# Kernel optimization log

Hardware: AMD Instinct MI355X
Metric: run time of the kernel (lower is better)

Reference implementation:

```python
import jax, jax.numpy as jnp
import numpy as np

Z, H, M, N, Y = 128, 512, 256, 10, 4   # z_size, hidden, mem_vec, mem_size, y_dim
B, T = 2048, 32
SHIFT_IND = np.concatenate([np.roll(np.arange(N), s) for s in (-1, 0, 1)])  # [3*N]


def setup_inputs() -> dict:
    key = jax.random.key(0)
    ks = iter(jax.random.split(key, 48))
    def nrm(shape, s=0.05):
        return jax.random.normal(next(ks), shape, dtype=jnp.float32) * s
    d = {}
    d["z_seq"] = jax.random.normal(next(ks), (B, T, Z), dtype=jnp.float32)
    d["W_ih"] = nrm((4 * H, Z + M)); d["W_hh"] = nrm((4 * H, H))
    d["b_ih"] = jnp.zeros((4 * H,), jnp.float32); d["b_hh"] = jnp.zeros((4 * H,), jnp.float32)
    heads = {"read_key": M, "write_key": M, "erase": M, "add": M, "y": Y,
             "rks": 1, "wks": 1, "rig": 1, "wig": 1, "rsh": 3, "wsh": 3, "rshp": 1, "wshp": 1}
    for nm, o in heads.items():
        d["W_" + nm] = nrm((o, H)); d["b_" + nm] = jnp.zeros((o,), jnp.float32)
    d["memory_init"] = nrm((N, M))
    d["gamma"] = jnp.ones((Z,), jnp.float32)
    d["beta"] = jnp.zeros((Z,), jnp.float32)
    return d


def reference(z_seq, W_ih, W_hh, b_ih, b_hh,
              W_read_key, b_read_key, W_write_key, b_write_key,
              W_erase, b_erase, W_add, b_add, W_y, b_y,
              W_rks, b_rks, W_wks, b_wks, W_rig, b_rig, W_wig, b_wig,
              W_rsh, b_rsh, W_wsh, b_wsh, W_rshp, b_rshp, W_wshp, b_wshp,
              memory_init, gamma, beta):
    Bs, Ts = z_seq.shape[0], z_seq.shape[1]
    eps = 1e-8
    # context norm over the time axis (single task segment), unbiased var as torch
    mu = z_seq.mean(1, keepdims=True)
    sig = jnp.sqrt(z_seq.var(1, ddof=1, keepdims=True) + eps)
    z = (z_seq - mu) / sig * gamma + beta
    z_ext = jnp.concatenate([z, jnp.zeros((Bs, 1, Z), z.dtype)], axis=1)  # t == T step uses zero input
    shift_ind = jnp.asarray(SHIFT_IND)

    def lin(h, W, b):
        return h @ W.T + b

    def cos_sim(key_v, mem):  # key [B,M], mem [B,N,M] -> [B,N]
        dot = jnp.einsum('bm,bnm->bn', key_v, mem)
        kn = jnp.maximum(jnp.linalg.norm(key_v, axis=1, keepdims=True), eps)
        mn = jnp.maximum(jnp.linalg.norm(mem, axis=2), eps)
        return dot / (kn * mn)

    def address(key_v, strength, gate, shift_w, sharpen, w_prev, mem, use_interp):
        # content addressing (exp(s*sim)/sum == softmax), interpolation, circular shift, sharpening
        w = jax.nn.softmax(strength * cos_sim(key_v, mem), axis=1)      # [B,N]
        w = jnp.where(use_interp, gate * w + (1.0 - gate) * w_prev, w)
        w_sh = w[:, shift_ind].reshape(Bs, 3, N)                        # gather per shift
        w = jnp.einsum('bsn,bs->bn', w_sh, shift_w)
        wp = w ** sharpen
        return wp / wp.sum(1, keepdims=True)

    def step(carry, xs):
        h, c, read_vec, mem, w_read, w_write = carry
        z_t, t = xs
        lstm_in = jnp.concatenate([z_t, read_vec], axis=1)              # [B, Z+M]
        gates = lstm_in @ W_ih.T + b_ih + h @ W_hh.T + b_hh
        i, f, g, o = jnp.split(gates, 4, axis=1)
        c = jax.nn.sigmoid(f) * c + jax.nn.sigmoid(i) * jnp.tanh(g)
        h = jax.nn.sigmoid(o) * jnp.tanh(c)
        read_key = jnp.tanh(lin(h, W_read_key, b_read_key))
        write_key = jnp.tanh(lin(h, W_write_key, b_write_key))
        rks = jax.nn.softplus(lin(h, W_rks, b_rks))
        wks = jax.nn.softplus(lin(h, W_wks, b_wks))
        rig = jax.nn.sigmoid(lin(h, W_rig, b_rig))
        wig = jax.nn.sigmoid(lin(h, W_wig, b_wig))
        rsh = jax.nn.softmax(lin(h, W_rsh, b_rsh), axis=1)
        wsh = jax.nn.softmax(lin(h, W_wsh, b_wsh), axis=1)
        rshp = jax.nn.softplus(lin(h, W_rshp, b_rshp)) + 1.0
        wshp = jax.nn.softplus(lin(h, W_wshp, b_wshp)) + 1.0
        erase = jax.nn.sigmoid(lin(h, W_erase, b_erase))
        add = jnp.tanh(lin(h, W_add, b_add))
        y_lin = lin(h, W_y, b_y)
        # read (skipped at t==0; interpolation only for t>1)
        w_read_new = address(read_key, rks, rig, rsh, rshp, w_read, mem, t > 1)
        read_vec = jnp.where(t == 0, jnp.zeros((Bs, M), z_t.dtype),
                             jnp.einsum('bnm,bn->bm', mem, w_read_new))
        w_read = jnp.where(t == 0, w_read, w_read_new)
        # write (every step; interpolation only for t>0)
        w_write = address(write_key, wks, wig, wsh, wshp, w_write, mem, t > 0)
        ww = w_write[:, :, None]
        mem = mem * (1.0 - erase[:, None, :] * ww) + add[:, None, :] * ww
        return (h, c, read_vec, mem, w_read, w_write), y_lin

    carry0 = (jnp.zeros((Bs, H), z.dtype), jnp.zeros((Bs, H), z.dtype),
              jnp.zeros((Bs, M), z.dtype),
              jnp.broadcast_to(memory_init, (Bs, N, M)).astype(z.dtype),
              jnp.zeros((Bs, N), z.dtype), jnp.zeros((Bs, N), z.dtype))
    ts = jnp.arange(Ts + 1)
    _, ys = jax.lax.scan(step, carry0, (jnp.swapaxes(z_ext, 0, 1), ts))
    y_pred_linear = ys[-1]  # output of the final (t == T) step
    return y_pred_linear, jnp.argmax(y_pred_linear, axis=1)
```

## Files before the change

kernel.cpp:

```cpp
#include <hip/hip_runtime.h>
#include <hip/hip_bf16.h>

typedef __attribute__((ext_vector_type(8))) short short8;
typedef __attribute__((ext_vector_type(4))) float f32x4;

#define Bsz   2048
#define Tsz   32
#define Zsz   128
#define Hsz   512
#define Msz   256
#define Nsz   10
#define KDIM  896
#define NGATE 2048
#define NHEAD 1040
#define NHEADP 1152

#define ACT_S ((size_t)Bsz * 768)
#define ZPL_S ((size_t)33 * Bsz * 128)
#define WG_S  ((size_t)NGATE * KDIM)
#define WH_S  ((size_t)NHEADP * Hsz)

__device__ __forceinline__ float sigmoidf_(float x) { return 1.f / (1.f + expf(-x)); }
__device__ __forceinline__ float softplusf_(float x) { return x > 20.f ? x : log1pf(expf(x)); }

__device__ __forceinline__ float wave_sum(float v) {
#pragma unroll
    for (int m = 32; m >= 1; m >>= 1) v += __shfl_xor(v, m, 64);
    return v;
}

__device__ __forceinline__ void split3(float v, __hip_bfloat16& o1, __hip_bfloat16& o2, __hip_bfloat16& o3) {
    o1 = __float2bfloat16(v);
    float r = v - __bfloat162float(o1);
    o2 = __float2bfloat16(r);
    r -= __bfloat162float(o2);
    o3 = __float2bfloat16(r);
}

__device__ __forceinline__ void split3u(float v, unsigned short& a, unsigned short& b, unsigned short& c) {
    __hip_bfloat16 x, y, z;
    split3(v, x, y, z);
    a = *reinterpret_cast<unsigned short*>(&x);
    b = *reinterpret_cast<unsigned short*>(&y);
    c = *reinterpret_cast<unsigned short*>(&z);
}

#define MFMA16(A, B, C) __builtin_amdgcn_mfma_f32_16x16x32_bf16((A), (B), (C), 0, 0, 0)

__device__ __forceinline__ void gload16(const void* g, void* l) {
    __builtin_amdgcn_global_load_lds(
        (const __attribute__((address_space(1))) void*)g,
        (__attribute__((address_space(3))) void*)l, 16, 0, 0);
}


__global__ __launch_bounds__(256) void k_lnorm(
    const float* __restrict__ z_seq, const float* __restrict__ gamma,
    const float* __restrict__ beta, __hip_bfloat16* __restrict__ zb)
{
    int idx = blockIdx.x * 256 + threadIdx.x;
    if (idx >= Bsz * Zsz) return;
    int b = idx >> 7, zi = idx & 127;
    const float* p = z_seq + (size_t)b * Tsz * Zsz + zi;
    float v[32];
    float s = 0.f;
#pragma unroll
    for (int t = 0; t < Tsz; t++) { v[t] = p[t * Zsz]; s += v[t]; }
    float mu = s * (1.f / 32.f);
    float ss = 0.f;
#pragma unroll
    for (int t = 0; t < Tsz; t++) { float d = v[t] - mu; ss += d * d; }
    float rs = rsqrtf(ss * (1.f / 31.f) + 1e-8f);
    float ga = gamma[zi], be = beta[zi];
#pragma unroll
    for (int t = 0; t <= Tsz; t++) {
        float val = (t < Tsz) ? (v[t] - mu) * rs * ga + be : 0.f;
        __hip_bfloat16 a, bq, c;
        split3(val, a, bq, c);
        size_t o = ((size_t)t * Bsz + b) * 128 + zi;
        zb[o] = a; zb[o + ZPL_S] = bq; zb[o + 2 * ZPL_S] = c;
    }
}

__global__ __launch_bounds__(256) void k_prep_wcat(
    const float* __restrict__ W_ih, const float* __restrict__ W_hh,
    const float* __restrict__ b_ih, const float* __restrict__ b_hh,
    __hip_bfloat16* __restrict__ Wt, float* __restrict__ bcat)
{
    int idx = blockIdx.x * 256 + threadIdx.x;
    if (idx >= NGATE * KDIM) return;
    int n = idx / KDIM, k = idx % KDIM;
    int jl = n & 15, g = (n >> 4) & 3, jg = n >> 6;
    int r = g * Hsz + jg * 16 + jl;
    float v = (k < 384) ? W_ih[(size_t)r * 384 + k] : W_hh[(size_t)r * Hsz + (k - 384)];
    __hip_bfloat16 a, b, c;
    split3(v, a, b, c);
    Wt[idx] = a; Wt[idx + WG_S] = b; Wt[idx + 2 * WG_S] = c;
    if (k == 0) bcat[n] = b_ih[r] + b_hh[r];
}

struct HeadP { const float* W[13]; const float* b[13]; };

__global__ __launch_bounds__(256) void k_prep_heads(
    HeadP hp, __hip_bfloat16* __restrict__ Wt, float* __restrict__ bh)
{
    int idx = blockIdx.x * 256 + threadIdx.x;
    if (idx >= NHEADP * Hsz) return;
    int n = idx / Hsz, k = idx % Hsz;
    float v = 0.f;
    if (n < NHEAD) {
        const int offs[14] = {0,256,512,768,1024,1028,1029,1030,1031,1032,1035,1038,1039,1040};
        int h = 0;
        while (n >= offs[h + 1]) h++;
        int local = n - offs[h];
        v = hp.W[h][(size_t)local * Hsz + k];
        if (k == 0) bh[n] = hp.b[h][local];
    } else if (k == 0) bh[n] = 0.f;
    __hip_bfloat16 a, b, c;
    split3(v, a, b, c);
    Wt[idx] = a; Wt[idx + WH_S] = b; Wt[idx + 2 * WH_S] = c;
}

__global__ __launch_bounds__(256) void k_init(
    __hip_bfloat16* __restrict__ act,
    float* __restrict__ cbuf, float* __restrict__ w_read, float* __restrict__ w_write,
    float* __restrict__ mem, const float* __restrict__ memory_init)
{
    int tid = blockIdx.x * blockDim.x + threadIdx.x;
    int stride = gridDim.x * blockDim.x;
    const __hip_bfloat16 z0 = __float2bfloat16(0.f);
    for (size_t i = tid; i < 6 * ACT_S; i += stride) act[i] = z0;
    for (int i = tid; i < Bsz * Hsz; i += stride) cbuf[i] = 0.f;
    for (int i = tid; i < Bsz * Nsz; i += stride) { w_read[i] = 0.f; w_write[i] = 0.f; }
    for (int i = tid; i < Bsz * Nsz * Msz; i += stride) mem[i] = memory_init[i % (Nsz * Msz)];
}


__device__ __forceinline__ void stage_tile(
    uint8_t* smem, int wid, int lane,
    const __hip_bfloat16* aP0, size_t aPlaneStride, int aRowStride, int aColOff, int row0,
    const __hip_bfloat16* bP0, size_t bPlaneStride, int bRowStride, int n00,
    int k0)
{
    const int row4 = lane >> 2;
    const int sch = (lane & 3) ^ (row4 & 3);
    const int koff = sch << 3;
#pragma unroll
    for (int i = 0; i < 9; ++i) {
        int c = wid * 9 + i;
        if (c < 24) {
            int p = c >> 3, rg = c & 7;
            int row = rg * 16 + row4;
            const __hip_bfloat16* g = aP0 + (size_t)p * aPlaneStride +
                (size_t)(row0 + row) * aRowStride + aColOff + k0 + koff;
            gload16(g, smem + p * 8192 + rg * 1024);
        } else {
            int c2 = c - 24;
            int p = c2 >> 2, rg = c2 & 3;
            int row = rg * 16 + row4;
            const __hip_bfloat16* g = bP0 + (size_t)p * bPlaneStride +
                (size_t)(n00 + row) * bRowStride + k0 + koff;
            gload16(g, smem + 24576 + p * 4096 + rg * 1024);
        }
    }
}

__global__ __launch_bounds__(256, 2) void k_gates(
    const __hip_bfloat16* __restrict__ zt,
    const __hip_bfloat16* __restrict__ actin,
    const __hip_bfloat16* __restrict__ Wg,
    const float* __restrict__ bcat,
    float* __restrict__ cbuf,
    __hip_bfloat16* __restrict__ actout)
{
    __shared__ __align__(1024) uint8_t smem[36864];
    const int tid = threadIdx.x;
    const int wid = tid >> 6, lane = tid & 63;
    const int fr = lane & 15, kg = lane >> 4;
    const int wr = wid >> 1, wc = wid & 1;
    const int wg = blockIdx.x;
    const int xcd = wg & 7, rr = wg >> 3;
    const int bm = (xcd & 1) * 8 + (rr & 7);
    const int bn = (xcd >> 1) * 8 + (rr >> 3);
    const int row0 = bm * 128, n00 = bn * 64;

    f32x4 acc[4][2];
#pragma unroll
    for (int s = 0; s < 4; ++s)
#pragma unroll
        for (int u = 0; u < 2; ++u) acc[s][u] = f32x4{0.f, 0.f, 0.f, 0.f};

    const int swz = (kg ^ (fr & 3)) << 4;
    constexpr int PA[6] = {0, 0, 1, 0, 1, 2};
    constexpr int PB[6] = {0, 1, 0, 2, 1, 0};

    const int NKT = KDIM / 32;
    for (int kt = 0; kt < NKT; ++kt) {
        const int k0 = kt * 32;
        if (k0 < 128)
            stage_tile(smem, wid, lane, zt, ZPL_S, 128, 0, row0, Wg, WG_S, KDIM, n00, k0);
        else
            stage_tile(smem, wid, lane, actin, ACT_S, 768, -128, row0, Wg, WG_S, KDIM, n00, k0);
        __syncthreads();

        short8 af[3][4];
#pragma unroll
        for (int p = 0; p < 3; ++p)
#pragma unroll
            for (int s = 0; s < 4; ++s)
                af[p][s] = *(const short8*)(smem + p * 8192 + (wr * 64 + s * 16 + fr) * 64 + swz);
        short8 bf[3][2];
#pragma unroll
        for (int p = 0; p < 3; ++p)
#pragma unroll
            for (int u = 0; u < 2; ++u)
                bf[p][u] = *(const short8*)(smem + 24576 + p * 4096 + (wc * 32 + u * 16 + fr) * 64 + swz);

#pragma unroll
        for (int pr = 0; pr < 6; ++pr)
#pragma unroll
            for (int s = 0; s < 4; ++s)
#pragma unroll
                for (int u = 0; u < 2; ++u)
                    acc[s][u] = MFMA16(af[PA[pr]][s], bf[PB[pr]][u], acc[s][u]);
        __syncthreads();
    }

    float* G = (float*)smem;
#pragma unroll
    for (int s = 0; s < 4; ++s)
#pragma unroll
        for (int u = 0; u < 2; ++u) {
            int g = wc * 2 + u;
#pragma unroll
            for (int r = 0; r < 4; ++r) {
                int row = wr * 64 + s * 16 + kg * 4 + r;
                G[(g * 128 + row) * 17 + fr] = acc[s][u][r];
            }
        }
    __syncthreads();

#pragma unroll
    for (int i = 0; i < 8; ++i) {
        int p2 = i * 256 + tid;
        int row = p2 >> 4, jl = p2 & 15;
        int m = row0 + row;
        int j = bn * 16 + jl;
        float iv = G[(0 * 128 + row) * 17 + jl] + bcat[n00 +  0 + jl];
        float fv = G[(1 * 128 + row) * 17 + jl] + bcat[n00 + 16 + jl];
        float gv = G[(2 * 128 + row) * 17 + jl] + bcat[n00 + 32 + jl];
        float ov = G[(3 * 128 + row) * 17 + jl] + bcat[n00 + 48 + jl];
        size_t ci = (size_t)m * Hsz + j;
        float co = cbuf[ci];
        float cn = sigmoidf_(fv) * co + sigmoidf_(iv) * tanhf(gv);
        float hn = sigmoidf_(ov) * tanhf(cn);
        cbuf[ci] = cn;
        __hip_bfloat16 h1, h2, h3;
        split3(hn, h1, h2, h3);
        size_t ho = (size_t)m * 768 + 256 + j;
        actout[ho] = h1; actout[ho + ACT_S] = h2; actout[ho + 2 * ACT_S] = h3;
    }
}

__global__ __launch_bounds__(256, 2) void k_heads(
    const __hip_bfloat16* __restrict__ actout,
    const __hip_bfloat16* __restrict__ Wh,
    const float* __restrict__ bh,
    float* __restrict__ headbuf,
    int nOff)
{
    __shared__ __align__(1024) uint8_t smem[36864];
    const int tid = threadIdx.x;
    const int wid = tid >> 6, lane = tid & 63;
    const int fr = lane & 15, kg = lane >> 4;
    const int wr = wid >> 1, wc = wid & 1;
    const int bm = blockIdx.x, bn = blockIdx.y + nOff;
    const int row0 = bm * 128, n00 = bn * 64;

    f32x4 acc[4][2];
#pragma unroll
    for (int s = 0; s < 4; ++s)
#pragma unroll
        for (int u = 0; u < 2; ++u) acc[s][u] = f32x4{0.f, 0.f, 0.f, 0.f};

    const int swz = (kg ^ (fr & 3)) << 4;
    constexpr int PA[6] = {0, 0, 1, 0, 1, 2};
    constexpr int PB[6] = {0, 1, 0, 2, 1, 0};

    const int NKT = Hsz / 32;
    for (int kt = 0; kt < NKT; ++kt) {
        stage_tile(smem, wid, lane, actout, ACT_S, 768, 256, row0, Wh, WH_S, Hsz, n00, kt * 32);
        __syncthreads();

        short8 af[3][4];
#pragma unroll
        for (int p = 0; p < 3; ++p)
#pragma unroll
            for (int s = 0; s < 4; ++s)
                af[p][s] = *(const short8*)(smem + p * 8192 + (wr * 64 + s * 16 + fr) * 64 + swz);
        short8 bf[3][2];
#pragma unroll
        for (int p = 0; p < 3; ++p)
#pragma unroll
            for (int u = 0; u < 2; ++u)
                bf[p][u] = *(const short8*)(smem + 24576 + p * 4096 + (wc * 32 + u * 16 + fr) * 64 + swz);

#pragma unroll
        for (int pr = 0; pr < 6; ++pr)
#pragma unroll
            for (int s = 0; s < 4; ++s)
#pragma unroll
                for (int u = 0; u < 2; ++u)
                    acc[s][u] = MFMA16(af[PA[pr]][s], bf[PB[pr]][u], acc[s][u]);
        __syncthreads();
    }

#pragma unroll
    for (int s = 0; s < 4; ++s)
#pragma unroll
        for (int u = 0; u < 2; ++u) {
            int n = n00 + wc * 32 + u * 16 + fr;
            if (n >= NHEAD) continue;
            float bias = bh[n];
#pragma unroll
            for (int r = 0; r < 4; ++r) {
                int m = row0 + wr * 64 + s * 16 + kg * 4 + r;
                headbuf[(size_t)m * NHEAD + n] = acc[s][u][r] + bias;
            }
        }
}


__device__ inline void compute_address(
    const float dot[10], const float mn[10], float kn, float strength, float gate,
    const float sh[3], float sharp, const float* __restrict__ wprev, bool interp,
    float out[10])
{
    float w[10];
    float mx = -1e30f;
#pragma unroll
    for (int n = 0; n < 10; n++) {
        w[n] = strength * (dot[n] / (kn * mn[n]));
        mx = fmaxf(mx, w[n]);
    }
    float s = 0.f;
#pragma unroll
    for (int n = 0; n < 10; n++) { w[n] = expf(w[n] - mx); s += w[n]; }
    float inv = 1.f / s;
#pragma unroll
    for (int n = 0; n < 10; n++) w[n] *= inv;
    if (interp) {
#pragma unroll
        for (int n = 0; n < 10; n++) w[n] = gate * w[n] + (1.f - gate) * wprev[n];
    }
    float w2[10];
#pragma unroll
    for (int n = 0; n < 10; n++) {
        int np1 = (n + 1) % 10, nm1 = (n + 9) % 10;
        w2[n] = sh[0] * w[np1] + sh[1] * w[n] + sh[2] * w[nm1];
    }
    float ssum = 0.f;
#pragma unroll
    for (int n = 0; n < 10; n++) { w2[n] = powf(w2[n], sharp); ssum += w2[n]; }
    float rinv = 1.f / ssum;
#pragma unroll
    for (int n = 0; n < 10; n++) out[n] = w2[n] * rinv;
}

__global__ __launch_bounds__(64) void k_addr3(
    const float* __restrict__ headbuf,
    float* __restrict__ mem,
    float* __restrict__ w_read, float* __restrict__ w_write,
    __hip_bfloat16* __restrict__ actout,
    int t)
{
    const int b = blockIdx.x;
    const int lane = threadIdx.x;
    const float eps = 1e-8f;
    const float* hb = headbuf + (size_t)b * NHEAD;
    float* memb = mem + (size_t)b * Nsz * Msz;

    float4 rk = *reinterpret_cast<const float4*>(hb + lane * 4);
    float4 wk = *reinterpret_cast<const float4*>(hb + 256 + lane * 4);
    float4 er = *reinterpret_cast<const float4*>(hb + 512 + lane * 4);
    float4 ad = *reinterpret_cast<const float4*>(hb + 768 + lane * 4);
    float4 mreg[10];
#pragma unroll
    for (int n = 0; n < 10; n++)
        mreg[n] = *reinterpret_cast<const float4*>(memb + n * Msz + lane * 4);

    rk.x = tanhf(rk.x); rk.y = tanhf(rk.y); rk.z = tanhf(rk.z); rk.w = tanhf(rk.w);
    wk.x = tanhf(wk.x); wk.y = tanhf(wk.y); wk.z = tanhf(wk.z); wk.w = tanhf(wk.w);
    er.x = sigmoidf_(er.x); er.y = sigmoidf_(er.y); er.z = sigmoidf_(er.z); er.w = sigmoidf_(er.w);
    ad.x = tanhf(ad.x); ad.y = tanhf(ad.y); ad.z = tanhf(ad.z); ad.w = tanhf(ad.w);

    float knr = fmaxf(sqrtf(wave_sum(rk.x*rk.x + rk.y*rk.y + rk.z*rk.z + rk.w*rk.w)), eps);
    float knw = fmaxf(sqrtf(wave_sum(wk.x*wk.x + wk.y*wk.y + wk.z*wk.z + wk.w*wk.w)), eps);

    float dotr[10], dotw[10], mn[10];
#pragma unroll
    for (int n = 0; n < 10; n++) {
        float4 m4 = mreg[n];
        dotr[n] = wave_sum(rk.x*m4.x + rk.y*m4.y + rk.z*m4.z + rk.w*m4.w);
        dotw[n] = wave_sum(wk.x*m4.x + wk.y*m4.y + wk.z*m4.z + wk.w*m4.w);
        mn[n]   = fmaxf(sqrtf(wave_sum(m4.x*m4.x + m4.y*m4.y + m4.z*m4.z + m4.w*m4.w)), eps);
    }

    float rks = softplusf_(hb[1028]);
    float wks = softplusf_(hb[1029]);
    float rig = sigmoidf_(hb[1030]);
    float wig = sigmoidf_(hb[1031]);
    float rsh[3], wsh[3];
    {
        float a0 = hb[1032], a1 = hb[1033], a2 = hb[1034];
        float mx = fmaxf(a0, fmaxf(a1, a2));
        float e0 = expf(a0 - mx), e1 = expf(a1 - mx), e2 = expf(a2 - mx);
        float inv = 1.f / (e0 + e1 + e2);
        rsh[0] = e0 * inv; rsh[1] = e1 * inv; rsh[2] = e2 * inv;
        a0 = hb[1035]; a1 = hb[1036]; a2 = hb[1037];
        mx = fmaxf(a0, fmaxf(a1, a2));
        e0 = expf(a0 - mx); e1 = expf(a1 - mx); e2 = expf(a2 - mx);
        inv = 1.f / (e0 + e1 + e2);
        wsh[0] = e0 * inv; wsh[1] = e1 * inv; wsh[2] = e2 * inv;
    }
    float rshp = softplusf_(hb[1038]) + 1.f;
    float wshp = softplusf_(hb[1039]) + 1.f;

    float wfr[10], wfw[10];
    compute_address(dotr, mn, knr, rks, rig, rsh, rshp, w_read + (size_t)b * Nsz, t > 1, wfr);
    compute_address(dotw, mn, knw, wks, wig, wsh, wshp, w_write + (size_t)b * Nsz, t > 0, wfw);

    {
        float4 rv = {0.f, 0.f, 0.f, 0.f};
#pragma unroll
        for (int n = 0; n < 10; n++) {
            float wn = wfr[n];
            rv.x += mreg[n].x * wn; rv.y += mreg[n].y * wn;
            rv.z += mreg[n].z * wn; rv.w += mreg[n].w * wn;
        }
        if (t == 0) rv = float4{0.f, 0.f, 0.f, 0.f};
        ushort4 u1, u2, u3;
        split3u(rv.x, u1.x, u2.x, u3.x);
        split3u(rv.y, u1.y, u2.y, u3.y);
        split3u(rv.z, u1.z, u2.z, u3.z);
        split3u(rv.w, u1.w, u2.w, u3.w);
        size_t o = (size_t)b * 768 + lane * 4;
        *reinterpret_cast<ushort4*>(actout + o)             = u1;
        *reinterpret_cast<ushort4*>(actout + o + ACT_S)     = u2;
        *reinterpret_cast<ushort4*>(actout + o + 2 * ACT_S) = u3;
    }
    if (lane < 10) {
        if (t != 0) w_read[(size_t)b * Nsz + lane] = wfr[lane];
        w_write[(size_t)b * Nsz + lane] = wfw[lane];
    }
#pragma unroll
    for (int n = 0; n < 10; n++) {
        float wwn = wfw[n];
        float4 m4 = mreg[n];
        float4 o4;
        o4.x = m4.x * (1.f - er.x * wwn) + ad.x * wwn;
        o4.y = m4.y * (1.f - er.y * wwn) + ad.y * wwn;
        o4.z = m4.z * (1.f - er.z * wwn) + ad.z * wwn;
        o4.w = m4.w * (1.f - er.w * wwn) + ad.w * wwn;
        *reinterpret_cast<float4*>(memb + n * Msz + lane * 4) = o4;
    }
}

__global__ __launch_bounds__(64) void k_out(
    const float* __restrict__ headbuf, float* __restrict__ d_out)
{
    int b = blockIdx.x * 64 + threadIdx.x;
    if (b >= Bsz) return;
    float4 y = *reinterpret_cast<const float4*>(headbuf + (size_t)b * NHEAD + 1024);
    d_out[(size_t)b * 4 + 0] = y.x;
    d_out[(size_t)b * 4 + 1] = y.y;
    d_out[(size_t)b * 4 + 2] = y.z;
    d_out[(size_t)b * 4 + 3] = y.w;
    int idx = 0; float best = y.x;
    if (y.y > best) { best = y.y; idx = 1; }
    if (y.z > best) { best = y.z; idx = 2; }
    if (y.w > best) { best = y.w; idx = 3; }
    d_out[Bsz * 4 + b] = (float)idx;
}


extern "C" void kernel_launch(void* const* d_in, const int* in_sizes, int n_in,
                              void* d_out, int out_size, void* d_ws, size_t ws_size,
                              hipStream_t stream) {
    const float* z_seq = (const float*)d_in[0];
    const float* W_ih  = (const float*)d_in[1];
    const float* W_hh  = (const float*)d_in[2];
    const float* b_ih  = (const float*)d_in[3];
    const float* b_hh  = (const float*)d_in[4];
    const float* memory_init = (const float*)d_in[31];
    const float* gamma = (const float*)d_in[32];
    const float* beta  = (const float*)d_in[33];

    HeadP hp;
    for (int i = 0; i < 13; i++) {
        hp.W[i] = (const float*)d_in[5 + 2 * i];
        hp.b[i] = (const float*)d_in[6 + 2 * i];
    }

    char* ws = (char*)d_ws;
    size_t off = 0;
    auto alloc = [&](size_t bytes) -> void* {
        off = (off + 255) & ~(size_t)255;
        void* p = ws + off;
        off += bytes;
        return p;
    };
    __hip_bfloat16* zbuf  = (__hip_bfloat16*)alloc(3 * ZPL_S * 2);
    __hip_bfloat16* act   = (__hip_bfloat16*)alloc(2 * 3 * ACT_S * 2);
    float* cbuf    = (float*)alloc((size_t)Bsz * Hsz * 4);
    float* mem     = (float*)alloc((size_t)Bsz * Nsz * Msz * 4);
    float* w_read  = (float*)alloc((size_t)Bsz * Nsz * 4);
    float* w_write = (float*)alloc((size_t)Bsz * Nsz * 4);
    float* headbuf = (float*)alloc((size_t)Bsz * NHEAD * 4);
    __hip_bfloat16* Wg = (__hip_bfloat16*)alloc(3 * WG_S * 2);
    float* bcat    = (float*)alloc((size_t)NGATE * 4);
    __hip_bfloat16* Wh = (__hip_bfloat16*)alloc(3 * WH_S * 2);
    float* bhead   = (float*)alloc((size_t)NHEADP * 4);

    k_prep_wcat<<<(NGATE * KDIM + 255) / 256, 256, 0, stream>>>(W_ih, W_hh, b_ih, b_hh, Wg, bcat);
    k_prep_heads<<<(NHEADP * Hsz + 255) / 256, 256, 0, stream>>>(hp, Wh, bhead);
    k_lnorm<<<(Bsz * Zsz + 255) / 256, 256, 0, stream>>>(z_seq, gamma, beta, zbuf);
    k_init<<<2048, 256, 0, stream>>>(act, cbuf, w_read, w_write, mem, memory_init);

    float* out_f = (float*)d_out;
    for (int t = 0; t < Tsz; t++) {
        const __hip_bfloat16* ain = act + (size_t)(t & 1) * 3 * ACT_S;
        __hip_bfloat16*       aout = act + (size_t)((t + 1) & 1) * 3 * ACT_S;
        k_gates<<<512, 256, 0, stream>>>(
            zbuf + (size_t)t * Bsz * 128, ain, Wg, bcat, cbuf, aout);
        k_heads<<<dim3(16, 18), 256, 0, stream>>>(aout, Wh, bhead, headbuf, 0);
        k_addr3<<<Bsz, 64, 0, stream>>>(headbuf, mem, w_read, w_write, aout, t);
    }
    {
        const int t = Tsz;
        const __hip_bfloat16* ain = act + (size_t)(t & 1) * 3 * ACT_S;
        __hip_bfloat16*       aout = act + (size_t)((t + 1) & 1) * 3 * ACT_S;
        k_gates<<<512, 256, 0, stream>>>(
            zbuf + (size_t)t * Bsz * 128, ain, Wg, bcat, cbuf, aout);
        k_heads<<<dim3(16, 1), 256, 0, stream>>>(aout, Wh, bhead, headbuf, 16);
        k_out<<<Bsz / 64, 64, 0, stream>>>(headbuf, out_f);
    }
}
```

Baseline: 3.409 ms.

## Split memory addressing kernel across four waves per batch row

The per-batch addressing kernel now runs 256 threads (four wavefronts) per batch element instead of one. Each wave holds two or three memory slots, computes partial dot products and norms, and exchanges them through shared memory. Wave 0 then computes the addressing weights, and all waves apply the erase/add update and partial read vectors, which are reduced in shared memory. The goal is more parallelism and fewer serial wave reductions per wave, at the cost of three block barriers and idle waves during the serial addressing step.

```diff
diff --git a/kernel.cpp b/kernel.cpp
--- a/kernel.cpp
+++ b/kernel.cpp
@@ -367,7 +367,7 @@
     for (int n = 0; n < 10; n++) out[n] = w2[n] * rinv;
 }
 
-__global__ __launch_bounds__(64) void k_addr3(
+__global__ __launch_bounds__(256) void k_addr4(
     const float* __restrict__ headbuf,
     float* __restrict__ mem,
     float* __restrict__ w_read, float* __restrict__ w_write,
@@ -375,69 +375,128 @@
     int t)
 {
     const int b = blockIdx.x;
-    const int lane = threadIdx.x;
+    const int tid = threadIdx.x;
+    const int wid = tid >> 6, lane = tid & 63;
     const float eps = 1e-8f;
     const float* hb = headbuf + (size_t)b * NHEAD;
     float* memb = mem + (size_t)b * Nsz * Msz;
+
+    __shared__ float fin[32];
+    __shared__ float W2[20];
+    __shared__ float4 Prv[4][64];
 
     float4 rk = *reinterpret_cast<const float4*>(hb + lane * 4);
     float4 wk = *reinterpret_cast<const float4*>(hb + 256 + lane * 4);
     float4 er = *reinterpret_cast<const float4*>(hb + 512 + lane * 4);
     float4 ad = *reinterpret_cast<const float4*>(hb + 768 + lane * 4);
-    float4 mreg[10];
-#pragma unroll
-    for (int n = 0; n < 10; n++)
-        mreg[n] = *reinterpret_cast<const float4*>(memb + n * Msz + lane * 4);
+
+    const int nc = (wid < 2) ? 3 : 2;
+    float4 mreg[3];
+#pragma unroll 3
+    for (int i = 0; i < 3; ++i) {
+        if (i < nc) {
+            int n = wid + i * 4;
+            mreg[i] = *reinterpret_cast<const float4*>(memb + n * Msz + lane * 4);
+        }
+    }
 
     rk.x = tanhf(rk.x); rk.y = tanhf(rk.y); rk.z = tanhf(rk.z); rk.w = tanhf(rk.w);
     wk.x = tanhf(wk.x); wk.y = tanhf(wk.y); wk.z = tanhf(wk.z); wk.w = tanhf(wk.w);
     er.x = sigmoidf_(er.x); er.y = sigmoidf_(er.y); er.z = sigmoidf_(er.z); er.w = sigmoidf_(er.w);
     ad.x = tanhf(ad.x); ad.y = tanhf(ad.y); ad.z = tanhf(ad.z); ad.w = tanhf(ad.w);
 
-    float knr = fmaxf(sqrtf(wave_sum(rk.x*rk.x + rk.y*rk.y + rk.z*rk.z + rk.w*rk.w)), eps);
-    float knw = fmaxf(sqrtf(wave_sum(wk.x*wk.x + wk.y*wk.y + wk.z*wk.z + wk.w*wk.w)), eps);
-
-    float dotr[10], dotw[10], mn[10];
-#pragma unroll
-    for (int n = 0; n < 10; n++) {
-        float4 m4 = mreg[n];
-        dotr[n] = wave_sum(rk.x*m4.x + rk.y*m4.y + rk.z*m4.z + rk.w*m4.w);
-        dotw[n] = wave_sum(wk.x*m4.x + wk.y*m4.y + wk.z*m4.z + wk.w*m4.w);
-        mn[n]   = fmaxf(sqrtf(wave_sum(m4.x*m4.x + m4.y*m4.y + m4.z*m4.z + m4.w*m4.w)), eps);
-    }
-
-    float rks = softplusf_(hb[1028]);
-    float wks = softplusf_(hb[1029]);
-    float rig = sigmoidf_(hb[1030]);
-    float wig = sigmoidf_(hb[1031]);
-    float rsh[3], wsh[3];
-    {
-        float a0 = hb[1032], a1 = hb[1033], a2 = hb[1034];
-        float mx = fmaxf(a0, fmaxf(a1, a2));
-        float e0 = expf(a0 - mx), e1 = expf(a1 - mx), e2 = expf(a2 - mx);
-        float inv = 1.f / (e0 + e1 + e2);
-        rsh[0] = e0 * inv; rsh[1] = e1 * inv; rsh[2] = e2 * inv;
-        a0 = hb[1035]; a1 = hb[1036]; a2 = hb[1037];
-        mx = fmaxf(a0, fmaxf(a1, a2));
-        e0 = expf(a0 - mx); e1 = expf(a1 - mx); e2 = expf(a2 - mx);
-        inv = 1.f / (e0 + e1 + e2);
-        wsh[0] = e0 * inv; wsh[1] = e1 * inv; wsh[2] = e2 * inv;
-    }
-    float rshp = softplusf_(hb[1038]) + 1.f;
-    float wshp = softplusf_(hb[1039]) + 1.f;
-
-    float wfr[10], wfw[10];
-    compute_address(dotr, mn, knr, rks, rig, rsh, rshp, w_read + (size_t)b * Nsz, t > 1, wfr);
-    compute_address(dotw, mn, knw, wks, wig, wsh, wshp, w_write + (size_t)b * Nsz, t > 0, wfw);
-
-    {
-        float4 rv = {0.f, 0.f, 0.f, 0.f};
+#pragma unroll 3
+    for (int i = 0; i < 3; ++i) {
+        if (i < nc) {
+            int n = wid + i * 4;
+            float4 m4 = mreg[i];
+            float dr = wave_sum(rk.x*m4.x + rk.y*m4.y + rk.z*m4.z + rk.w*m4.w);
+            float dw = wave_sum(wk.x*m4.x + wk.y*m4.y + wk.z*m4.z + wk.w*m4.w);
+            float m2 = wave_sum(m4.x*m4.x + m4.y*m4.y + m4.z*m4.z + m4.w*m4.w);
+            if (lane == 0) { fin[n] = dr; fin[10 + n] = dw; fin[20 + n] = m2; }
+        }
+    }
+    if (wid == 0) {
+        float k2r = wave_sum(rk.x*rk.x + rk.y*rk.y + rk.z*rk.z + rk.w*rk.w);
+        if (lane == 0) fin[30] = k2r;
+    } else if (wid == 1) {
+        float k2w = wave_sum(wk.x*wk.x + wk.y*wk.y + wk.z*wk.z + wk.w*wk.w);
+        if (lane == 0) fin[31] = k2w;
+    }
+    __syncthreads();
+
+    if (wid == 0) {
+        float dotr[10], dotw[10], mn[10];
 #pragma unroll
         for (int n = 0; n < 10; n++) {
-            float wn = wfr[n];
-            rv.x += mreg[n].x * wn; rv.y += mreg[n].y * wn;
-            rv.z += mreg[n].z * wn; rv.w += mreg[n].w * wn;
-        }
+            dotr[n] = fin[n];
+            dotw[n] = fin[10 + n];
+            mn[n] = fmaxf(sqrtf(fin[20 + n]), eps);
+        }
+        const float knr = fmaxf(sqrtf(fin[30]), eps);
+        const float knw = fmaxf(sqrtf(fin[31]), eps);
+
+        float rks = softplusf_(hb[1028]);
+        float wks = softplusf_(hb[1029]);
+        float rig = sigmoidf_(hb[1030]);
+        float wig = sigmoidf_(hb[1031]);
+        float rsh[3], wsh[3];
+        {
+            float a0 = hb[1032], a1 = hb[1033], a2 = hb[1034];
+            float mx = fmaxf(a0, fmaxf(a1, a2));
+            float e0 = expf(a0 - mx), e1 = expf(a1 - mx), e2 = expf(a2 - mx);
+            float inv = 1.f / (e0 + e1 + e2);
+            rsh[0] = e0 * inv; rsh[1] = e1 * inv; rsh[2] = e2 * inv;
+            a0 = hb[1035]; a1 = hb[1036]; a2 = hb[1037];
+            mx = fmaxf(a0, fmaxf(a1, a2));
+            e0 = expf(a0 - mx); e1 = expf(a1 - mx); e2 = expf(a2 - mx);
+            inv = 1.f / (e0 + e1 + e2);
+            wsh[0] = e0 * inv; wsh[1] = e1 * inv; wsh[2] = e2 * inv;
+        }
+        float rshp = softplusf_(hb[1038]) + 1.f;
+        float wshp = softplusf_(hb[1039]) + 1.f;
+
+        float wfr[10], wfw[10];
+        compute_address(dotr, mn, knr, rks, rig, rsh, rshp, w_read + (size_t)b * Nsz, t > 1, wfr);
+        compute_address(dotw, mn, knw, wks, wig, wsh, wshp, w_write + (size_t)b * Nsz, t > 0, wfw);
+
+        if (lane < 10) {
+            W2[lane] = wfr[lane];
+            W2[10 + lane] = wfw[lane];
+            if (t != 0) w_read[(size_t)b * Nsz + lane] = wfr[lane];
+            w_write[(size_t)b * Nsz + lane] = wfw[lane];
+        }
+    }
+    __syncthreads();
+
+    float4 rvp = {0.f, 0.f, 0.f, 0.f};
+#pragma unroll 3
+    for (int i = 0; i < 3; ++i) {
+        if (i < nc) {
+            int n = wid + i * 4;
+            float wfrn = W2[n];
+            float wwn = W2[10 + n];
+            float4 m4 = mreg[i];
+            rvp.x += m4.x * wfrn; rvp.y += m4.y * wfrn;
+            rvp.z += m4.z * wfrn; rvp.w += m4.w * wfrn;
+            float4 o4;
+            o4.x = m4.x * (1.f - er.x * wwn) + ad.x * wwn;
+            o4.y = m4.y * (1.f - er.y * wwn) + ad.y * wwn;
+            o4.z = m4.z * (1.f - er.z * wwn) + ad.z * wwn;
+            o4.w = m4.w * (1.f - er.w * wwn) + ad.w * wwn;
+            *reinterpret_cast<float4*>(memb + n * Msz + lane * 4) = o4;
+        }
+    }
+    Prv[wid][lane] = rvp;
+    __syncthreads();
+
+    if (wid == 0) {
+        float4 p0 = Prv[0][lane], p1 = Prv[1][lane], p2 = Prv[2][lane], p3 = Prv[3][lane];
+        float4 rv;
+        rv.x = (p0.x + p1.x) + (p2.x + p3.x);
+        rv.y = (p0.y + p1.y) + (p2.y + p3.y);
+        rv.z = (p0.z + p1.z) + (p2.z + p3.z);
+        rv.w = (p0.w + p1.w) + (p2.w + p3.w);
         if (t == 0) rv = float4{0.f, 0.f, 0.f, 0.f};
         ushort4 u1, u2, u3;
         split3u(rv.x, u1.x, u2.x, u3.x);
@@ -448,21 +507,6 @@
         *reinterpret_cast<ushort4*>(actout + o)             = u1;
         *reinterpret_cast<ushort4*>(actout + o + ACT_S)     = u2;
         *reinterpret_cast<ushort4*>(actout + o + 2 * ACT_S) = u3;
-    }
-    if (lane < 10) {
-        if (t != 0) w_read[(size_t)b * Nsz + lane] = wfr[lane];
-        w_write[(size_t)b * Nsz + lane] = wfw[lane];
-    }
-#pragma unroll
-    for (int n = 0; n < 10; n++) {
-        float wwn = wfw[n];
-        float4 m4 = mreg[n];
-        float4 o4;
-        o4.x = m4.x * (1.f - er.x * wwn) + ad.x * wwn;
-        o4.y = m4.y * (1.f - er.y * wwn) + ad.y * wwn;
-        o4.z = m4.z * (1.f - er.z * wwn) + ad.z * wwn;
-        o4.w = m4.w * (1.f - er.w * wwn) + ad.w * wwn;
-        *reinterpret_cast<float4*>(memb + n * Msz + lane * 4) = o4;
     }
 }
 
@@ -534,7 +578,7 @@
         k_gates<<<512, 256, 0, stream>>>(
             zbuf + (size_t)t * Bsz * 128, ain, Wg, bcat, cbuf, aout);
         k_heads<<<dim3(16, 18), 256, 0, stream>>>(aout, Wh, bhead, headbuf, 0);
-        k_addr3<<<Bsz, 64, 0, stream>>>(headbuf, mem, w_read, w_write, aout, t);
+        k_addr4<<<Bsz, 256, 0, stream>>>(headbuf, mem, w_read, w_write, aout, t);
     }
     {
         const int t = Tsz;
```

After: 3.764 ms. 10.4% more time.

## Fuse per-step kernels into one persistent cooperative kernel with grid syncs

Applied to the files above, without the earlier changes.

Replaces the per-timestep launches of the gates, heads and addressing kernels with a single cooperative persistent kernel. Stages are separated by grid-wide barriers, and the blocks loop over the tiles and rows of each stage. This removes roughly a hundred kernel launches and their launch gaps. In exchange it adds grid-sync costs, and the addressing stage packs four 64-lane rows into each 256-thread block at the GEMM kernel's occupancy. The old multi-launch path is kept as a fallback if the cooperative launch fails.

```diff
diff --git a/kernel.cpp b/kernel.cpp
--- a/kernel.cpp
+++ b/kernel.cpp
@@ -1,5 +1,8 @@
 #include <hip/hip_runtime.h>
 #include <hip/hip_bf16.h>
+#include <hip/hip_cooperative_groups.h>
+
+namespace cg = cooperative_groups;
 
 typedef __attribute__((ext_vector_type(8))) short short8;
 typedef __attribute__((ext_vector_type(4))) float f32x4;
@@ -165,7 +168,8 @@
     }
 }
 
-__global__ __launch_bounds__(256, 2) void k_gates(
+__device__ void gates_tile(
+    uint8_t* smem, int wg,
     const __hip_bfloat16* __restrict__ zt,
     const __hip_bfloat16* __restrict__ actin,
     const __hip_bfloat16* __restrict__ Wg,
@@ -173,12 +177,10 @@
     float* __restrict__ cbuf,
     __hip_bfloat16* __restrict__ actout)
 {
-    __shared__ __align__(1024) uint8_t smem[36864];
     const int tid = threadIdx.x;
     const int wid = tid >> 6, lane = tid & 63;
     const int fr = lane & 15, kg = lane >> 4;
     const int wr = wid >> 1, wc = wid & 1;
-    const int wg = blockIdx.x;
     const int xcd = wg & 7, rr = wg >> 3;
     const int bm = (xcd & 1) * 8 + (rr & 7);
     const int bn = (xcd >> 1) * 8 + (rr >> 3);
@@ -260,21 +262,21 @@
         size_t ho = (size_t)m * 768 + 256 + j;
         actout[ho] = h1; actout[ho + ACT_S] = h2; actout[ho + 2 * ACT_S] = h3;
     }
-}
-
-__global__ __launch_bounds__(256, 2) void k_heads(
+    __syncthreads();
+}
+
+__device__ void heads_tile(
+    uint8_t* smem,
     const __hip_bfloat16* __restrict__ actout,
     const __hip_bfloat16* __restrict__ Wh,
     const float* __restrict__ bh,
     float* __restrict__ headbuf,
-    int nOff)
-{
-    __shared__ __align__(1024) uint8_t smem[36864];
+    int bm, int bn)
+{
     const int tid = threadIdx.x;
     const int wid = tid >> 6, lane = tid & 63;
     const int fr = lane & 15, kg = lane >> 4;
     const int wr = wid >> 1, wc = wid & 1;
-    const int bm = blockIdx.x, bn = blockIdx.y + nOff;
     const int row0 = bm * 128, n00 = bn * 64;
 
     f32x4 acc[4][2];
@@ -328,10 +330,10 @@
                 headbuf[(size_t)m * NHEAD + n] = acc[s][u][r] + bias;
             }
         }
-}
-
-
-__device__ inline void compute_address(
+    __syncthreads();
+}
+
+__device__ void compute_address(
     const float dot[10], const float mn[10], float kn, float strength, float gate,
     const float sh[3], float sharp, const float* __restrict__ wprev, bool interp,
     float out[10])
@@ -367,15 +369,13 @@
     for (int n = 0; n < 10; n++) out[n] = w2[n] * rinv;
 }
 
-__global__ __launch_bounds__(64) void k_addr3(
+__device__ void addr_row(
     const float* __restrict__ headbuf,
     float* __restrict__ mem,
     float* __restrict__ w_read, float* __restrict__ w_write,
     __hip_bfloat16* __restrict__ actout,
-    int t)
-{
-    const int b = blockIdx.x;
-    const int lane = threadIdx.x;
+    int t, int b, int lane)
+{
     const float eps = 1e-8f;
     const float* hb = headbuf + (size_t)b * NHEAD;
     float* memb = mem + (size_t)b * Nsz * Msz;
@@ -466,6 +466,32 @@
     }
 }
 
+
+__global__ __launch_bounds__(256, 2) void k_gates(
+    const __hip_bfloat16* __restrict__ zt, const __hip_bfloat16* __restrict__ actin,
+    const __hip_bfloat16* __restrict__ Wg, const float* __restrict__ bcat,
+    float* __restrict__ cbuf, __hip_bfloat16* __restrict__ actout)
+{
+    __shared__ __align__(1024) uint8_t smem[36864];
+    gates_tile(smem, blockIdx.x, zt, actin, Wg, bcat, cbuf, actout);
+}
+
+__global__ __launch_bounds__(256, 2) void k_heads(
+    const __hip_bfloat16* __restrict__ actout, const __hip_bfloat16* __restrict__ Wh,
+    const float* __restrict__ bh, float* __restrict__ headbuf, int nOff)
+{
+    __shared__ __align__(1024) uint8_t smem[36864];
+    heads_tile(smem, actout, Wh, bh, headbuf, blockIdx.x, blockIdx.y + nOff);
+}
+
+__global__ __launch_bounds__(64) void k_addr3(
+    const float* __restrict__ headbuf, float* __restrict__ mem,
+    float* __restrict__ w_read, float* __restrict__ w_write,
+    __hip_bfloat16* __restrict__ actout, int t)
+{
+    addr_row(headbuf, mem, w_read, w_write, actout, t, blockIdx.x, threadIdx.x);
+}
+
 __global__ __launch_bounds__(64) void k_out(
     const float* __restrict__ headbuf, float* __restrict__ d_out)
 {
@@ -481,6 +507,70 @@
     if (y.z > best) { best = y.z; idx = 2; }
     if (y.w > best) { best = y.w; idx = 3; }
     d_out[Bsz * 4 + b] = (float)idx;
+}
+
+
+__global__ __launch_bounds__(256, 2) void k_step_all(
+    const __hip_bfloat16* __restrict__ zbuf,
+    __hip_bfloat16* __restrict__ act,
+    const __hip_bfloat16* __restrict__ Wg,
+    const float* __restrict__ bcat,
+    float* __restrict__ cbuf,
+    const __hip_bfloat16* __restrict__ Wh,
+    const float* __restrict__ bhead,
+    float* __restrict__ headbuf,
+    float* __restrict__ mem,
+    float* __restrict__ w_read,
+    float* __restrict__ w_write,
+    float* __restrict__ d_out)
+{
+    cg::grid_group grid = cg::this_grid();
+    __shared__ __align__(1024) uint8_t smem[36864];
+    const int tid = threadIdx.x;
+    const int wid = tid >> 6, lane = tid & 63;
+    const int bid = blockIdx.x;
+    const int nb = gridDim.x;
+
+    for (int t = 0; t <= Tsz; ++t) {
+        const __hip_bfloat16* ain = act + (size_t)(t & 1) * 3 * ACT_S;
+        __hip_bfloat16*       aout = act + (size_t)((t + 1) & 1) * 3 * ACT_S;
+        const __hip_bfloat16* zt = zbuf + (size_t)t * Bsz * 128;
+
+        for (int wg = bid; wg < 512; wg += nb)
+            gates_tile(smem, wg, zt, ain, Wg, bcat, cbuf, aout);
+        __threadfence();
+        grid.sync();
+
+        if (t < Tsz) {
+            for (int i = bid; i < 288; i += nb)
+                heads_tile(smem, aout, Wh, bhead, headbuf, i & 15, i >> 4);
+            __threadfence();
+            grid.sync();
+
+            for (int r = bid * 4 + wid; r < Bsz; r += nb * 4)
+                addr_row(headbuf, mem, w_read, w_write, aout, t, r, lane);
+            __threadfence();
+            grid.sync();
+        } else {
+            for (int i = bid; i < 16; i += nb)
+                heads_tile(smem, aout, Wh, bhead, headbuf, i, 16);
+            __threadfence();
+            grid.sync();
+
+            for (int b = bid * 256 + tid; b < Bsz; b += nb * 256) {
+                float4 y = *reinterpret_cast<const float4*>(headbuf + (size_t)b * NHEAD + 1024);
+                d_out[(size_t)b * 4 + 0] = y.x;
+                d_out[(size_t)b * 4 + 1] = y.y;
+                d_out[(size_t)b * 4 + 2] = y.z;
+                d_out[(size_t)b * 4 + 3] = y.w;
+                int idx = 0; float best = y.x;
+                if (y.y > best) { best = y.y; idx = 1; }
+                if (y.z > best) { best = y.z; idx = 2; }
+                if (y.w > best) { best = y.w; idx = 3; }
+                d_out[Bsz * 4 + b] = (float)idx;
+            }
+        }
+    }
 }
 
 
@@ -528,15 +618,33 @@
     k_init<<<2048, 256, 0, stream>>>(act, cbuf, w_read, w_write, mem, memory_init);
 
     float* out_f = (float*)d_out;
-    for (int t = 0; t < Tsz; t++) {
-        const __hip_bfloat16* ain = act + (size_t)(t & 1) * 3 * ACT_S;
-        __hip_bfloat16*       aout = act + (size_t)((t + 1) & 1) * 3 * ACT_S;
-        k_gates<<<512, 256, 0, stream>>>(
-            zbuf + (size_t)t * Bsz * 128, ain, Wg, bcat, cbuf, aout);
-        k_heads<<<dim3(16, 18), 256, 0, stream>>>(aout, Wh, bhead, headbuf, 0);
-        k_addr3<<<Bsz, 64, 0, stream>>>(headbuf, mem, w_read, w_write, aout, t);
-    }
-    {
+
+    int maxActive = 0;
+    hipError_t qe = hipOccupancyMaxActiveBlocksPerMultiprocessor(
+        &maxActive, (const void*)k_step_all, 256, 0);
+    bool coop_done = false;
+    if (qe == hipSuccess && maxActive >= 1) {
+        int nblk = (maxActive >= 2) ? 512 : 256;
+        void* args[] = {
+            (void*)&zbuf, (void*)&act, (void*)&Wg, (void*)&bcat, (void*)&cbuf,
+            (void*)&Wh, (void*)&bhead, (void*)&headbuf, (void*)&mem,
+            (void*)&w_read, (void*)&w_write, (void*)&out_f
+        };
+        hipError_t le = hipLaunchCooperativeKernel((const void*)k_step_all,
+                                                   dim3(nblk), dim3(256), args, 0, stream);
+        if (le == hipSuccess) coop_done = true;
+        else (void)hipGetLastError();
+    }
+
+    if (!coop_done) {
+        for (int t = 0; t < Tsz; t++) {
+            const __hip_bfloat16* ain = act + (size_t)(t & 1) * 3 * ACT_S;
+            __hip_bfloat16*       aout = act + (size_t)((t + 1) & 1) * 3 * ACT_S;
+            k_gates<<<512, 256, 0, stream>>>(
+                zbuf + (size_t)t * Bsz * 128, ain, Wg, bcat, cbuf, aout);
+            k_heads<<<dim3(16, 18), 256, 0, stream>>>(aout, Wh, bhead, headbuf, 0);
+            k_addr3<<<Bsz, 64, 0, stream>>>(headbuf, mem, w_read, w_write, aout, t);
+        }
         const int t = Tsz;
         const __hip_bfloat16* ain = act + (size_t)(t & 1) * 3 * ACT_S;
         __hip_bfloat16*       aout = act + (size_t)((t + 1) & 1) * 3 * ACT_S;
```

New measurement: 4.878 ms. 43.1% more time.

## Skip zero-state GEMM work at first step, drop act zeroing, swizzle heads tiles

Applied to the files above, without the earlier changes.

At t=0 the gates GEMM runs only over the z input columns (4 k-tiles), because the recurrent state and read vector are zero then. This lets the initial zero-fill of the activation buffers be dropped. The heads kernel also remaps block indices so tiles sharing operands land on the same XCD, aiming for better L2 reuse. The risk is that any activation region later read without being written first, such as the read-vector slice of the second buffer, now holds uninitialised data.

```diff
diff --git a/kernel.cpp b/kernel.cpp
--- a/kernel.cpp
+++ b/kernel.cpp
@@ -122,14 +122,11 @@
 }
 
 __global__ __launch_bounds__(256) void k_init(
-    __hip_bfloat16* __restrict__ act,
     float* __restrict__ cbuf, float* __restrict__ w_read, float* __restrict__ w_write,
     float* __restrict__ mem, const float* __restrict__ memory_init)
 {
     int tid = blockIdx.x * blockDim.x + threadIdx.x;
     int stride = gridDim.x * blockDim.x;
-    const __hip_bfloat16 z0 = __float2bfloat16(0.f);
-    for (size_t i = tid; i < 6 * ACT_S; i += stride) act[i] = z0;
     for (int i = tid; i < Bsz * Hsz; i += stride) cbuf[i] = 0.f;
     for (int i = tid; i < Bsz * Nsz; i += stride) { w_read[i] = 0.f; w_write[i] = 0.f; }
     for (int i = tid; i < Bsz * Nsz * Msz; i += stride) mem[i] = memory_init[i % (Nsz * Msz)];
@@ -165,6 +162,7 @@
     }
 }
 
+template<int NKT>
 __global__ __launch_bounds__(256, 2) void k_gates(
     const __hip_bfloat16* __restrict__ zt,
     const __hip_bfloat16* __restrict__ actin,
@@ -194,7 +192,6 @@
     constexpr int PA[6] = {0, 0, 1, 0, 1, 2};
     constexpr int PB[6] = {0, 1, 0, 2, 1, 0};
 
-    const int NKT = KDIM / 32;
     for (int kt = 0; kt < NKT; ++kt) {
         const int k0 = kt * 32;
         if (k0 < 128)
@@ -274,7 +271,16 @@
     const int wid = tid >> 6, lane = tid & 63;
     const int fr = lane & 15, kg = lane >> 4;
     const int wr = wid >> 1, wc = wid & 1;
-    const int bm = blockIdx.x, bn = blockIdx.y + nOff;
+    int bm, bn;
+    if (nOff == 0) {
+        int lin = blockIdx.y * 16 + blockIdx.x;
+        int swz = (lin & 7) * 36 + (lin >> 3);
+        bm = swz & 15;
+        bn = swz >> 4;
+    } else {
+        bm = blockIdx.x;
+        bn = nOff;
+    }
     const int row0 = bm * 128, n00 = bn * 64;
 
     f32x4 acc[4][2];
@@ -283,7 +289,7 @@
 #pragma unroll
         for (int u = 0; u < 2; ++u) acc[s][u] = f32x4{0.f, 0.f, 0.f, 0.f};
 
-    const int swz = (kg ^ (fr & 3)) << 4;
+    const int swzl = (kg ^ (fr & 3)) << 4;
     constexpr int PA[6] = {0, 0, 1, 0, 1, 2};
     constexpr int PB[6] = {0, 1, 0, 2, 1, 0};
 
@@ -297,13 +303,13 @@
         for (int p = 0; p < 3; ++p)
 #pragma unroll
             for (int s = 0; s < 4; ++s)
-                af[p][s] = *(const short8*)(smem + p * 8192 + (wr * 64 + s * 16 + fr) * 64 + swz);
+                af[p][s] = *(const short8*)(smem + p * 8192 + (wr * 64 + s * 16 + fr) * 64 + swzl);
         short8 bf[3][2];
 #pragma unroll
         for (int p = 0; p < 3; ++p)
 #pragma unroll
             for (int u = 0; u < 2; ++u)
-                bf[p][u] = *(const short8*)(smem + 24576 + p * 4096 + (wc * 32 + u * 16 + fr) * 64 + swz);
+                bf[p][u] = *(const short8*)(smem + 24576 + p * 4096 + (wc * 32 + u * 16 + fr) * 64 + swzl);
 
 #pragma unroll
         for (int pr = 0; pr < 6; ++pr)
@@ -525,14 +531,18 @@
     k_prep_wcat<<<(NGATE * KDIM + 255) / 256, 256, 0, stream>>>(W_ih, W_hh, b_ih, b_hh, Wg, bcat);
     k_prep_heads<<<(NHEADP * Hsz + 255) / 256, 256, 0, stream>>>(hp, Wh, bhead);
     k_lnorm<<<(Bsz * Zsz + 255) / 256, 256, 0, stream>>>(z_seq, gamma, beta, zbuf);
-    k_init<<<2048, 256, 0, stream>>>(act, cbuf, w_read, w_write, mem, memory_init);
+    k_init<<<2048, 256, 0, stream>>>(cbuf, w_read, w_write, mem, memory_init);
 
     float* out_f = (float*)d_out;
     for (int t = 0; t < Tsz; t++) {
         const __hip_bfloat16* ain = act + (size_t)(t & 1) * 3 * ACT_S;
         __hip_bfloat16*       aout = act + (size_t)((t + 1) & 1) * 3 * ACT_S;
-        k_gates<<<512, 256, 0, stream>>>(
-            zbuf + (size_t)t * Bsz * 128, ain, Wg, bcat, cbuf, aout);
+        if (t == 0)
+            k_gates<4><<<512, 256, 0, stream>>>(
+                zbuf, ain, Wg, bcat, cbuf, aout);
+        else
+            k_gates<28><<<512, 256, 0, stream>>>(
+                zbuf + (size_t)t * Bsz * 128, ain, Wg, bcat, cbuf, aout);
         k_heads<<<dim3(16, 18), 256, 0, stream>>>(aout, Wh, bhead, headbuf, 0);
         k_addr3<<<Bsz, 64, 0, stream>>>(headbuf, mem, w_read, w_write, aout, t);
     }
@@ -540,7 +550,7 @@
         const int t = Tsz;
         const __hip_bfloat16* ain = act + (size_t)(t & 1) * 3 * ACT_S;
         __hip_bfloat16*       aout = act + (size_t)((t + 1) & 1) * 3 * ACT_S;
-        k_gates<<<512, 256, 0, stream>>>(
+        k_gates<28><<<512, 256, 0, stream>>>(
             zbuf + (size_t)t * Bsz * 128, ain, Wg, bcat, cbuf, aout);
         k_heads<<<dim3(16, 1), 256, 0, stream>>>(aout, Wh, bhead, headbuf, 16);
         k_out<<<Bsz / 64, 64, 0, stream>>>(headbuf, out_f);
```

After: 3.458 ms. Within noise of the previous version (+1.4%).
